# Kernel tuning notes

Measured on AMD Instinct MI355X. Metric: run time of the kernel, lower is better.

## Reference

```python
import jax, jax.numpy as jnp
import numpy as np

N_NODES = 50000
N_EDGES = 800000
D_IN = 256
D_HID = 256
N_CLASSES = 10
N_GRAPHS = 512
LN_EPS = 1e-5


def gcn_conv(x, edge_index, W, b, num_nodes):
    # PyG GCNConv (default settings): h = x @ W; add self-loops; symmetric
    # deg^{-1/2} normalization; sum-aggregate messages; add bias.
    h = x @ W                                   # [N, H]
    loop = jnp.arange(num_nodes, dtype=edge_index.dtype)
    src = jnp.concatenate([edge_index[0], loop])  # [E+N]
    dst = jnp.concatenate([edge_index[1], loop])  # [E+N]
    deg = jax.ops.segment_sum(jnp.ones_like(dst, dtype=h.dtype), dst,
                              num_segments=num_nodes)
    dinv = jnp.where(deg > 0, jax.lax.rsqrt(deg), 0.0)
    norm = dinv[src] * dinv[dst]                # [E+N]
    msg = h[src] * norm[:, None]                # gather + scale
    out = jax.ops.segment_sum(msg, dst, num_segments=num_nodes)  # scatter-add
    return out + b


def layer_norm(x, w, b):
    mu = jnp.mean(x, axis=-1, keepdims=True)
    var = jnp.mean(jnp.square(x - mu), axis=-1, keepdims=True)
    return (x - mu) * jax.lax.rsqrt(var + LN_EPS) * w + b


def global_mean_pool(x, batch, num_graphs):
    s = jax.ops.segment_sum(x, batch, num_segments=num_graphs)
    cnt = jax.ops.segment_sum(jnp.ones_like(batch, dtype=x.dtype), batch,
                              num_segments=num_graphs)
    return s / jnp.maximum(cnt, 1.0)[:, None]


def setup_inputs() -> dict:
    key = jax.random.key(0)
    ks = jax.random.split(key, 12)
    x = jax.random.normal(ks[0], (N_NODES, D_IN), dtype=jnp.float32)
    edge_index = jax.random.randint(ks[1], (2, N_EDGES), 0, N_NODES, dtype=jnp.int32)
    batch = jnp.sort(jax.random.randint(ks[2], (N_NODES,), 0, N_GRAPHS, dtype=jnp.int32))
    s_in = 1.0 / np.sqrt(D_IN)
    s_hid = 1.0 / np.sqrt(D_HID)
    return {
        "x": x,
        "edge_index": edge_index,
        "batch": batch,
        "W1": jax.random.uniform(ks[3], (D_IN, D_HID), jnp.float32, -s_in, s_in),
        "b1": jnp.zeros((D_HID,), jnp.float32),
        "W2": jax.random.uniform(ks[4], (D_HID, D_HID), jnp.float32, -s_hid, s_hid),
        "b2": jnp.zeros((D_HID,), jnp.float32),
        "ln1_w": jnp.ones((D_HID,), jnp.float32),
        "ln1_b": jnp.zeros((D_HID,), jnp.float32),
        "ln2_w": jnp.ones((D_HID,), jnp.float32),
        "ln2_b": jnp.zeros((D_HID,), jnp.float32),
        "lin_W": jax.random.uniform(ks[5], (D_HID, N_CLASSES), jnp.float32, -s_hid, s_hid),
        "lin_b": jnp.zeros((N_CLASSES,), jnp.float32),
    }


def reference(x, edge_index, batch, W1, b1, W2, b2, ln1_w, ln1_b, ln2_w, ln2_b, lin_W, lin_b):
    # dropout is identity at inference (training=False)
    h = gcn_conv(x, edge_index, W1, b1, N_NODES)
    h = jax.nn.relu(layer_norm(h, ln1_w, ln1_b))
    h = gcn_conv(h, edge_index, W2, b2, N_NODES)
    h = jax.nn.relu(layer_norm(h, ln2_w, ln2_b))
    pooled = global_mean_pool(h, batch, N_GRAPHS)   # [G, H]
    return pooled @ lin_W + lin_b                   # [G, C]
```

## Files before the change

kernel.cpp:

```cpp
#include <hip/hip_runtime.h>
#include <hip/hip_fp8.h>
#include <stdint.h>

#define D 256
#define CAP 64
#define NBIN_CAP 8192

typedef __attribute__((ext_vector_type(8))) short short8;
typedef __attribute__((ext_vector_type(4))) float f32x4;

#define SW2(n, c) (((n) << 7) + ((((c) ^ ((n) & 7))) << 3))

__device__ inline unsigned short f2bf(float f) {
    uint32_t u = __builtin_bit_cast(uint32_t, f);
    uint32_t r = (u + 0x7FFFu + ((u >> 16) & 1u)) >> 16;
    return (unsigned short)r;
}

__device__ inline float bf2f(unsigned short b) {
    return __builtin_bit_cast(float, (uint32_t)b << 16);
}

__device__ inline f32x4 fp8x4_to_f32(uint32_t v) {
    __hip_fp8x4_e4m3 a;
    a.__x = v;
    float4 f = (float4)a;
    return (f32x4){f.x, f.y, f.z, f.w};
}

__device__ inline uint8_t f32_to_fp8(float f) {
    __hip_fp8_e4m3 q(f);
    return (uint8_t)q.__x;
}

__global__ __launch_bounds__(256) void k_prep(const float* __restrict__ x,
                                              unsigned short* __restrict__ xb, int n8,
                                              const float* __restrict__ W1,
                                              const float* __restrict__ W2,
                                              unsigned short* __restrict__ Wt1,
                                              unsigned short* __restrict__ Wt2,
                                              const int* __restrict__ src,
                                              const int* __restrict__ dst,
                                              int* __restrict__ gbin,
                                              uint32_t* __restrict__ binbuf,
                                              int ne, int nf2b) {
    __shared__ int hist[256];
    int b = blockIdx.x, t = threadIdx.x;
    if (b < nf2b) {
        int i = b * 256 + t;
        if (i < n8) {
            f32x4 v0 = ((const f32x4*)x)[i * 2];
            f32x4 v1 = ((const f32x4*)x)[i * 2 + 1];
            short8 o;
            o[0] = (short)f2bf(v0.x); o[1] = (short)f2bf(v0.y);
            o[2] = (short)f2bf(v0.z); o[3] = (short)f2bf(v0.w);
            o[4] = (short)f2bf(v1.x); o[5] = (short)f2bf(v1.y);
            o[6] = (short)f2bf(v1.z); o[7] = (short)f2bf(v1.w);
            ((short8*)xb)[i] = o;
        }
    } else if (b < nf2b + 512) {
        int idx = (b - nf2b) * 256 + t;
        int w = idx >> 16;
        int r = idx & 65535;
        int n = r >> 8, k = r & 255;
        const float* W = w ? W2 : W1;
        unsigned short* Wt = w ? Wt2 : Wt1;
        Wt[n * 256 + k] = f2bf(W[k * 256 + n]);
    } else {
        int fid = b - nf2b - 512;
        hist[t] = 0;
        __syncthreads();
        int e0 = fid * 4096;
#pragma unroll
        for (int j = 0; j < 16; ++j) {
            int i = e0 + j * 256 + t;
            if (i < ne) atomicAdd(&hist[dst[i] >> 8], 1);
        }
        __syncthreads();
        int h = hist[t];
        int base = (h > 0) ? atomicAdd(&gbin[t], h) : 0;
        hist[t] = base;
        __syncthreads();
#pragma unroll
        for (int j = 0; j < 16; ++j) {
            int i = e0 + j * 256 + t;
            if (i < ne) {
                int d = dst[i];
                int bn = d >> 8;
                int slot = atomicAdd(&hist[bn], 1);
                if (slot < NBIN_CAP)
                    binbuf[(size_t)bn * NBIN_CAP + slot] =
                        (uint32_t)src[i] | ((uint32_t)(d & 255) << 16);
            }
        }
    }
}


__device__ __forceinline__ void gemm_body(unsigned short* sm, int gid,
                                          const unsigned short* __restrict__ A,
                                          const unsigned short* __restrict__ Bt,
                                          uint8_t* __restrict__ Cb, int M) {
    int t = threadIdx.x;
    int wave = t >> 6, lane = t & 63;
    int quad = lane >> 4, l16 = lane & 15;
    int mr = wave >> 1, nc = wave & 1;
    int bm = (gid >> 1) * 128;
    int bn = (gid & 1) * 128;

    uint4 af[4][8];
#pragma unroll
    for (int tm = 0; tm < 4; ++tm) {
        int row = bm + mr * 64 + tm * 16 + l16;
        if (row >= M) row = M - 1;
        const unsigned short* ap = A + (size_t)row * D + quad * 8;
#pragma unroll
        for (int ks = 0; ks < 8; ++ks)
            af[tm][ks] = *reinterpret_cast<const uint4*>(ap + ks * 32);
    }

    f32x4 acc[4][4];
#pragma unroll
    for (int tm = 0; tm < 4; ++tm)
#pragma unroll
        for (int tn = 0; tn < 4; ++tn) acc[tm][tn] = (f32x4){0.f, 0.f, 0.f, 0.f};

#pragma unroll
    for (int half = 0; half < 2; ++half) {
        {
            int c = t & 15;
            int r0 = t >> 4;
#pragma unroll
            for (int j = 0; j < 8; ++j) {
                int r = r0 + j * 16;
                uint4 v = *reinterpret_cast<const uint4*>(
                    Bt + (size_t)(bn + r) * D + half * 128 + c * 8);
                *reinterpret_cast<uint4*>(sm + SW2(r, c)) = v;
            }
        }
        __syncthreads();
#pragma unroll
        for (int ks = 0; ks < 4; ++ks) {
            int gks = half * 4 + ks;
            short8 b[4];
#pragma unroll
            for (int tn = 0; tn < 4; ++tn) {
                int n = nc * 64 + tn * 16 + l16;
                b[tn] = *reinterpret_cast<const short8*>(sm + SW2(n, ks * 4 + quad));
            }
#pragma unroll
            for (int tm = 0; tm < 4; ++tm) {
                short8 a = __builtin_bit_cast(short8, af[tm][gks]);
#pragma unroll
                for (int tn = 0; tn < 4; ++tn)
                    acc[tm][tn] = __builtin_amdgcn_mfma_f32_16x16x32_bf16(a, b[tn], acc[tm][tn], 0, 0, 0);
            }
        }
        __syncthreads();
    }

    uint8_t (*sC)[136] = reinterpret_cast<uint8_t (*)[136]>(sm);
#pragma unroll
    for (int tm = 0; tm < 4; ++tm) {
        int rb = mr * 64 + tm * 16 + quad * 4;
#pragma unroll
        for (int tn = 0; tn < 4; ++tn) {
            int cc = nc * 64 + tn * 16 + l16;
#pragma unroll
            for (int r = 0; r < 4; ++r)
                sC[rb + r][cc] = f32_to_fp8(acc[tm][tn][r]);
        }
    }
    __syncthreads();

#pragma unroll
    for (int it = 0; it < 4; ++it) {
        int idx = it * 256 + t;
        int r = idx >> 3, ch = idx & 7;
        int gr = bm + r;
        if (gr < M)
            *reinterpret_cast<uint4*>(Cb + (size_t)gr * D + bn + ch * 16) =
                *reinterpret_cast<const uint4*>(&sC[r][ch * 16]);
    }
}

__device__ __forceinline__ void binB_body(unsigned short* sm, int bb,
                                          const uint32_t* __restrict__ binbuf,
                                          const int* __restrict__ gbin,
                                          unsigned short* __restrict__ ewi,
                                          int* __restrict__ cur, int nNodes) {
    __shared__ int lcur[256];
    int t = threadIdx.x;
    lcur[t] = 0;
    __syncthreads();
    int cnt = min(gbin[bb], NBIN_CAP);
    const uint32_t* bp = binbuf + (size_t)bb * NBIN_CAP;
    for (int i = t; i < cnt; i += 256) {
        uint32_t v = bp[i];
        int n = v >> 16;
        int p = atomicAdd(&lcur[n], 1);
        if (p < CAP) sm[n * CAP + p] = (unsigned short)(v & 0xFFFF);
    }
    __syncthreads();
    int node0 = bb * 256;
    int nvalid = min(256, nNodes - node0);
    int nch = nvalid * (CAP / 8);
    uint4* dstp = (uint4*)(ewi + (size_t)node0 * CAP);
    for (int i = t; i < nch; i += 256)
        dstp[i] = *reinterpret_cast<const uint4*>(sm + i * 8);
    if (t < nvalid) cur[node0 + t] = lcur[t];
}

__global__ __launch_bounds__(256, 2) void k_gemmfill(const unsigned short* __restrict__ A,
                                                     const unsigned short* __restrict__ Bt,
                                                     uint8_t* __restrict__ Cb, int M,
                                                     const uint32_t* __restrict__ binbuf,
                                                     const int* __restrict__ gbin,
                                                     unsigned short* __restrict__ ewi,
                                                     int* __restrict__ cur,
                                                     int NBI, int ngemm) {
    __shared__ unsigned short sm[16384];
    int b = blockIdx.x;
    if (b < 2 * NBI) {
        if (b & 1) binB_body(sm, b >> 1, binbuf, gbin, ewi, cur, M);
        else       gemm_body(sm, b >> 1, A, Bt, Cb, M);
    } else {
        int r = b - NBI;
        if (r < ngemm) gemm_body(sm, r, A, Bt, Cb, M);
        else           binB_body(sm, r - ngemm + NBI, binbuf, gbin, ewi, cur, M);
    }
}

__global__ __launch_bounds__(256, 2) void k_gemm(const unsigned short* __restrict__ A,
                                                 const unsigned short* __restrict__ Bt,
                                                 uint8_t* __restrict__ Cb, int M) {
    __shared__ unsigned short sm[16384];
    gemm_body(sm, blockIdx.x, A, Bt, Cb, M);
}

__global__ __launch_bounds__(256) void k_agg(const uint8_t* __restrict__ hb,
                                             const int* __restrict__ cur,
                                             const unsigned short* __restrict__ ewi,
                                             const float* __restrict__ bias,
                                             const float* __restrict__ lnw,
                                             const float* __restrict__ lnb,
                                             unsigned short* __restrict__ out, int n) {
    __shared__ int2 lew[4][CAP];
    int wave = threadIdx.x >> 6, lane = threadIdx.x & 63;
    int node = blockIdx.x * 4 + wave;
    if (node >= n) return;
    int cdeg = cur[node];
    int cnt = min(cdeg, CAP);
    if (lane < cnt) {
        int s = (int)ewi[(size_t)node * CAP + lane];
        int2 p;
        p.x = s * 64;
        p.y = __builtin_bit_cast(int, rsqrtf((float)(cur[s] + 1)));
        lew[wave][lane] = p;
    }
    __builtin_amdgcn_wave_barrier();

    float di = rsqrtf((float)(cdeg + 1));
    const uint32_t* hb32 = (const uint32_t*)hb;
    uint32_t rs = hb32[(uint32_t)node * 64 + lane];
    f32x4 acc = (f32x4){0.f, 0.f, 0.f, 0.f};
    const int2* lep = lew[wave];
    int nq = cnt >> 2;

    int2 p0, p1, p2, p3;
    if (nq > 0) { p0 = lep[0]; p1 = lep[1]; p2 = lep[2]; p3 = lep[3]; }
    int q = 0;
#pragma unroll 1
    for (; q + 1 < nq; ++q) {
        int b4 = (q + 1) * 4;
        uint32_t r0 = hb32[(uint32_t)(p0.x + lane)];
        uint32_t r1 = hb32[(uint32_t)(p1.x + lane)];
        uint32_t r2 = hb32[(uint32_t)(p2.x + lane)];
        uint32_t r3 = hb32[(uint32_t)(p3.x + lane)];
        int2 n0 = lep[b4], n1 = lep[b4 + 1], n2 = lep[b4 + 2], n3 = lep[b4 + 3];
        acc += fp8x4_to_f32(r0) * __builtin_bit_cast(float, p0.y);
        acc += fp8x4_to_f32(r1) * __builtin_bit_cast(float, p1.y);
        acc += fp8x4_to_f32(r2) * __builtin_bit_cast(float, p2.y);
        acc += fp8x4_to_f32(r3) * __builtin_bit_cast(float, p3.y);
        p0 = n0; p1 = n1; p2 = n2; p3 = n3;
    }
    if (nq > 0) {
        uint32_t r0 = hb32[(uint32_t)(p0.x + lane)];
        uint32_t r1 = hb32[(uint32_t)(p1.x + lane)];
        uint32_t r2 = hb32[(uint32_t)(p2.x + lane)];
        uint32_t r3 = hb32[(uint32_t)(p3.x + lane)];
        acc += fp8x4_to_f32(r0) * __builtin_bit_cast(float, p0.y);
        acc += fp8x4_to_f32(r1) * __builtin_bit_cast(float, p1.y);
        acc += fp8x4_to_f32(r2) * __builtin_bit_cast(float, p2.y);
        acc += fp8x4_to_f32(r3) * __builtin_bit_cast(float, p3.y);
    }
    for (int e = nq * 4; e < cnt; ++e) {
        int2 p = lep[e];
        uint32_t r = hb32[(uint32_t)(p.x + lane)];
        acc += fp8x4_to_f32(r) * __builtin_bit_cast(float, p.y);
    }

    f32x4 self = fp8x4_to_f32(rs);
    f32x4 b4v = ((const f32x4*)bias)[lane];
    f32x4 v = self * (di * di) + acc * di + b4v;

    float s1 = v.x + v.y + v.z + v.w;
    float s2 = v.x * v.x + v.y * v.y + v.z * v.z + v.w * v.w;
#pragma unroll
    for (int o = 32; o > 0; o >>= 1) {
        s1 += __shfl_xor(s1, o, 64);
        s2 += __shfl_xor(s2, o, 64);
    }
    float mean = s1 * (1.0f / 256.0f);
    float var = s2 * (1.0f / 256.0f) - mean * mean;
    float inv = rsqrtf(var + 1e-5f);
    f32x4 w4 = ((const f32x4*)lnw)[lane];
    f32x4 lb = ((const f32x4*)lnb)[lane];
    float y0 = fmaxf((v.x - mean) * inv * w4.x + lb.x, 0.f);
    float y1 = fmaxf((v.y - mean) * inv * w4.y + lb.y, 0.f);
    float y2 = fmaxf((v.z - mean) * inv * w4.z + lb.z, 0.f);
    float y3 = fmaxf((v.w - mean) * inv * w4.w + lb.w, 0.f);
    uint2 w;
    w.x = (uint32_t)f2bf(y0) | ((uint32_t)f2bf(y1) << 16);
    w.y = (uint32_t)f2bf(y2) | ((uint32_t)f2bf(y3) << 16);
    *reinterpret_cast<uint2*>(out + (size_t)node * D + lane * 4) = w;
}

__global__ __launch_bounds__(256) void k_pool(const unsigned short* __restrict__ h,
                                              const int* __restrict__ batch,
                                              const float* __restrict__ linW,
                                              const float* __restrict__ linb,
                                              float* __restrict__ out,
                                              int nNodes) {
    int g = blockIdx.x, t = threadIdx.x;
    int lo = 0, hi = nNodes;
    while (lo < hi) { int m = (lo + hi) >> 1; if (batch[m] < g) lo = m + 1; else hi = m; }
    int lo2 = lo, hi2 = nNodes;
    while (lo2 < hi2) { int m = (lo2 + hi2) >> 1; if (batch[m] < g + 1) lo2 = m + 1; else hi2 = m; }
    float s0 = 0.f, s1 = 0.f, s2 = 0.f, s3 = 0.f;
    int i = lo;
    for (; i + 4 <= lo2; i += 4) {
        s0 += bf2f(h[(size_t)(i + 0) * D + t]);
        s1 += bf2f(h[(size_t)(i + 1) * D + t]);
        s2 += bf2f(h[(size_t)(i + 2) * D + t]);
        s3 += bf2f(h[(size_t)(i + 3) * D + t]);
    }
    for (; i < lo2; ++i) s0 += bf2f(h[(size_t)i * D + t]);
    float s = (s0 + s1) + (s2 + s3);
    float cnt = (float)(lo2 - lo);
    float pooled = s / fmaxf(cnt, 1.f);
    __shared__ float sp[256];
    __shared__ float red[4];
    sp[t] = pooled;
    __syncthreads();
    for (int c = 0; c < 10; ++c) {
        float v = sp[t] * linW[t * 10 + c];
#pragma unroll
        for (int o = 32; o > 0; o >>= 1) v += __shfl_xor(v, o, 64);
        if ((t & 63) == 0) red[t >> 6] = v;
        __syncthreads();
        if (t == 0) out[g * 10 + c] = red[0] + red[1] + red[2] + red[3] + linb[c];
        __syncthreads();
    }
}

extern "C" void kernel_launch(void* const* d_in, const int* in_sizes, int n_in,
                              void* d_out, int out_size, void* d_ws, size_t ws_size,
                              hipStream_t stream) {
    const float* x    = (const float*)d_in[0];
    const int*   ei   = (const int*)d_in[1];
    const int*   batch= (const int*)d_in[2];
    const float* W1   = (const float*)d_in[3];
    const float* b1   = (const float*)d_in[4];
    const float* W2   = (const float*)d_in[5];
    const float* b2   = (const float*)d_in[6];
    const float* ln1w = (const float*)d_in[7];
    const float* ln1b = (const float*)d_in[8];
    const float* ln2w = (const float*)d_in[9];
    const float* ln2b = (const float*)d_in[10];
    const float* linW = (const float*)d_in[11];
    const float* linb = (const float*)d_in[12];
    float* out = (float*)d_out;

    int nNodes  = in_sizes[0] / D;
    int nEdges  = in_sizes[1] / 2;
    int nGraphs = out_size / 10;

    const int* src = ei;
    const int* dst = ei + nEdges;

    char* ws = (char*)d_ws;
    size_t o = 0;
    auto alloc = [&](size_t bytes) -> char* {
        char* p = ws + o;
        o += (bytes + 511) & ~(size_t)511;
        return p;
    };
    unsigned short* xb = (unsigned short*)alloc((size_t)nNodes * D * 2);
    uint8_t* hW = (uint8_t*)alloc((size_t)nNodes * D);
    unsigned short* h1 = (unsigned short*)alloc((size_t)nNodes * D * 2);
    int* cur   = (int*)alloc((size_t)nNodes * 4);
    unsigned short* ewi = (unsigned short*)alloc((size_t)nNodes * CAP * 2);
    unsigned short* Wt1 = (unsigned short*)alloc((size_t)D * D * 2);
    unsigned short* Wt2 = (unsigned short*)alloc((size_t)D * D * 2);

    int NB = (nNodes + 255) / 256;
    uint32_t* binbuf = (uint32_t*)alloc((size_t)NB * NBIN_CAP * 4);
    int* gbin = (int*)alloc((size_t)NB * 4);
    (void)ws_size;

    int ge = (nEdges + 4095) / 4096;
    int n8 = nNodes * (D / 8);
    int nf2b = (n8 + 255) / 256;
    int ngemm = ((nNodes + 127) / 128) * 2;
    int NBI = min(NB, ngemm);

    hipMemsetAsync(gbin, 0, (size_t)NB * 4, stream);
    k_prep<<<nf2b + 512 + ge, 256, 0, stream>>>(x, xb, n8, W1, W2, Wt1, Wt2,
                                                src, dst, gbin, binbuf,
                                                nEdges, nf2b);
    k_gemmfill<<<ngemm + NB, 256, 0, stream>>>(xb, Wt1, hW, nNodes,
                                               binbuf, gbin, ewi, cur,
                                               NBI, ngemm);
    k_agg<<<(nNodes + 3) / 4, 256, 0, stream>>>(hW, cur, ewi,
                                                b1, ln1w, ln1b, h1, nNodes);
    k_gemm<<<ngemm, 256, 0, stream>>>(h1, Wt2, hW, nNodes);
    k_agg<<<(nNodes + 3) / 4, 256, 0, stream>>>(hW, cur, ewi,
                                                b2, ln2w, ln2b, xb, nNodes);
    k_pool<<<nGraphs, 256, 0, stream>>>(xb, batch, linW, linb, out, nNodes);
}
```

Before: 269.6 us.

## Reorder prep kernel blocks, tile weight transpose via LDS, batch edge loads

The prep kernel now schedules the edge-binning blocks first so the latency-bound atomic work starts earliest. The weight transpose uses 64x64 LDS tiles with padding instead of strided per-element global reads. The x-to-bf16 cast handles four vectors per thread with fewer blocks. Edge src/dst are loaded once into registers rather than re-read between the two passes. This raises register and LDS use in the shared kernel, which may lower occupancy for every branch.

```diff
diff --git a/kernel.cpp b/kernel.cpp
--- a/kernel.cpp
+++ b/kernel.cpp
@@ -43,39 +43,24 @@
                                               const int* __restrict__ dst,
                                               int* __restrict__ gbin,
                                               uint32_t* __restrict__ binbuf,
-                                              int ne, int nf2b) {
+                                              int ne, int nA) {
     __shared__ int hist[256];
+    __shared__ unsigned short tile[64 * 66];
     int b = blockIdx.x, t = threadIdx.x;
-    if (b < nf2b) {
-        int i = b * 256 + t;
-        if (i < n8) {
-            f32x4 v0 = ((const f32x4*)x)[i * 2];
-            f32x4 v1 = ((const f32x4*)x)[i * 2 + 1];
-            short8 o;
-            o[0] = (short)f2bf(v0.x); o[1] = (short)f2bf(v0.y);
-            o[2] = (short)f2bf(v0.z); o[3] = (short)f2bf(v0.w);
-            o[4] = (short)f2bf(v1.x); o[5] = (short)f2bf(v1.y);
-            o[6] = (short)f2bf(v1.z); o[7] = (short)f2bf(v1.w);
-            ((short8*)xb)[i] = o;
-        }
-    } else if (b < nf2b + 512) {
-        int idx = (b - nf2b) * 256 + t;
-        int w = idx >> 16;
-        int r = idx & 65535;
-        int n = r >> 8, k = r & 255;
-        const float* W = w ? W2 : W1;
-        unsigned short* Wt = w ? Wt2 : Wt1;
-        Wt[n * 256 + k] = f2bf(W[k * 256 + n]);
-    } else {
-        int fid = b - nf2b - 512;
+    if (b < nA) {
+        int e0 = b * 4096;
+        int dv[16], sv[16];
         hist[t] = 0;
         __syncthreads();
-        int e0 = fid * 4096;
 #pragma unroll
         for (int j = 0; j < 16; ++j) {
             int i = e0 + j * 256 + t;
-            if (i < ne) atomicAdd(&hist[dst[i] >> 8], 1);
-        }
+            dv[j] = (i < ne) ? dst[i] : -1;
+            sv[j] = (i < ne) ? src[i] : 0;
+        }
+#pragma unroll
+        for (int j = 0; j < 16; ++j)
+            if (dv[j] >= 0) atomicAdd(&hist[dv[j] >> 8], 1);
         __syncthreads();
         int h = hist[t];
         int base = (h > 0) ? atomicAdd(&gbin[t], h) : 0;
@@ -83,14 +68,47 @@
         __syncthreads();
 #pragma unroll
         for (int j = 0; j < 16; ++j) {
-            int i = e0 + j * 256 + t;
-            if (i < ne) {
-                int d = dst[i];
-                int bn = d >> 8;
+            if (dv[j] >= 0) {
+                int bn = dv[j] >> 8;
                 int slot = atomicAdd(&hist[bn], 1);
                 if (slot < NBIN_CAP)
                     binbuf[(size_t)bn * NBIN_CAP + slot] =
-                        (uint32_t)src[i] | ((uint32_t)(d & 255) << 16);
+                        (uint32_t)sv[j] | ((uint32_t)(dv[j] & 255) << 16);
+            }
+        }
+    } else if (b < nA + 32) {
+        int tr = b - nA;
+        int w = tr >> 4;
+        const float* W = w ? W2 : W1;
+        unsigned short* Wt = w ? Wt2 : Wt1;
+        int tid = tr & 15;
+        int kr = (tid >> 2) * 64, nc = (tid & 3) * 64;
+        int lane = t & 63, grp = t >> 6;
+#pragma unroll
+        for (int j = 0; j < 16; ++j) {
+            int rl = grp * 16 + j;
+            tile[rl * 66 + lane] = f2bf(W[(kr + rl) * 256 + nc + lane]);
+        }
+        __syncthreads();
+#pragma unroll
+        for (int j = 0; j < 16; ++j) {
+            int rl = grp * 16 + j;
+            Wt[(size_t)(nc + rl) * 256 + kr + lane] = tile[lane * 66 + rl];
+        }
+    } else {
+        int i0 = (b - nA - 32) * 1024 + t;
+#pragma unroll
+        for (int j = 0; j < 4; ++j) {
+            int i = i0 + j * 256;
+            if (i < n8) {
+                f32x4 v0 = ((const f32x4*)x)[i * 2];
+                f32x4 v1 = ((const f32x4*)x)[i * 2 + 1];
+                short8 o;
+                o[0] = (short)f2bf(v0.x); o[1] = (short)f2bf(v0.y);
+                o[2] = (short)f2bf(v0.z); o[3] = (short)f2bf(v0.w);
+                o[4] = (short)f2bf(v1.x); o[5] = (short)f2bf(v1.y);
+                o[6] = (short)f2bf(v1.z); o[7] = (short)f2bf(v1.w);
+                ((short8*)xb)[i] = o;
             }
         }
     }
@@ -409,16 +427,16 @@
     int* gbin = (int*)alloc((size_t)NB * 4);
     (void)ws_size;
 
-    int ge = (nEdges + 4095) / 4096;
+    int nA = (nEdges + 4095) / 4096;
     int n8 = nNodes * (D / 8);
-    int nf2b = (n8 + 255) / 256;
+    int ncast = (n8 + 1023) / 1024;
     int ngemm = ((nNodes + 127) / 128) * 2;
     int NBI = min(NB, ngemm);
 
     hipMemsetAsync(gbin, 0, (size_t)NB * 4, stream);
-    k_prep<<<nf2b + 512 + ge, 256, 0, stream>>>(x, xb, n8, W1, W2, Wt1, Wt2,
+    k_prep<<<nA + 32 + ncast, 256, 0, stream>>>(x, xb, n8, W1, W2, Wt1, Wt2,
                                                 src, dst, gbin, binbuf,
-                                                nEdges, nf2b);
+                                                nEdges, nA);
     k_gemmfill<<<ngemm + NB, 256, 0, stream>>>(xb, Wt1, hW, nNodes,
                                                binbuf, gbin, ewi, cur,
                                                NBI, ngemm);
```

New measurement: 259.6 us. 1.04x faster.
